# Kernel optimization log

Measured on AMD Instinct MI355X. Metric: run time of the kernel, lower is better.

## Reference

```python
import jax, jax.numpy as jnp
import numpy as np

B, T, A, F, K, DQ, DV = 64, 1024, 128, 1024, 31, 1024, 512  # filters F == T required by source math


def setup_inputs() -> dict:
    key = jax.random.key(0)
    ks = jax.random.split(key, 8)
    s = 0.05
    return {
        "query": jax.random.normal(ks[0], (B, 1, DQ), jnp.float32),
        "value": jax.random.normal(ks[1], (B, T, DV), jnp.float32),
        "attention_weights_cat": jax.random.uniform(ks[2], (B, T, 2), jnp.float32),
        "Wq": jax.random.normal(ks[3], (DQ, A), jnp.float32) * s,
        "Wm": jax.random.normal(ks[4], (DV, A), jnp.float32) * s,
        "Wv": jax.random.normal(ks[5], (A, 1), jnp.float32) * s,
        "Wconv": jax.random.normal(ks[6], (K, 2, F), jnp.float32) * s,
        "Wloc": jax.random.normal(ks[7], (T, A), jnp.float32) * s,
    }


def reference(query, value, attention_weights_cat, Wq, Wm, Wv, Wconv, Wloc):
    # query_layer: Dense(tanh, no bias): [B,1,DQ] -> [B,1,A]
    q = jnp.tanh(jnp.einsum('bld,da->bla', query, Wq))
    # memory_layer: Dense(tanh, no bias): [B,T,DV] -> [B,T,A]
    v = jnp.tanh(jnp.einsum('btd,da->bta', value, Wm))
    # location conv (SAME, no bias): [B,T,2] -> [B,T,F]
    loc = jax.lax.conv_general_dilated(
        attention_weights_cat, Wconv, window_strides=(1,), padding='SAME',
        dimension_numbers=('NWC', 'WIO', 'NWC'))
    # source transposes [0,2,1] then Dense(T->A, tanh): [B,F,T] -> [B,F,A]
    loc = jnp.tanh(jnp.einsum('bft,ta->bfa', jnp.transpose(loc, (0, 2, 1)), Wloc))
    # additive score (F == T so broadcast add is element-aligned): [B,T,1]
    score = jnp.einsum('bta,ao->bto', jnp.tanh(q + v + loc), Wv)
    alignment = jax.nn.softmax(score, axis=1)                # softmax over time
    context = jnp.sum(alignment * v, axis=1)                  # [B,A]
    return context, jnp.transpose(alignment, (0, 2, 1))       # [B,1,T]
```

## Files before the change

### kernel.cpp

```cpp
#include <hip/hip_runtime.h>
#include <hip/hip_bf16.h>

#define BB 64
#define TT 1024
#define AA 128
#define FF 1024
#define DQ 1024
#define DV 512

typedef __bf16 bf16x8_t __attribute__((ext_vector_type(8)));
typedef __bf16 bf16x4_t __attribute__((ext_vector_type(4)));
typedef float f32x4_t __attribute__((ext_vector_type(4)));
typedef _Float16 f16x4_t __attribute__((ext_vector_type(4)));

__device__ __forceinline__ float ftanh(float x) {
    float e = __expf(2.0f * x);
    return 1.0f - 2.0f / (e + 1.0f);
}

__device__ __forceinline__ __bf16 bhi(float x) { return (__bf16)x; }
__device__ __forceinline__ __bf16 blo(float x) {
    __bf16 h = (__bf16)x;
    return (__bf16)(x - (float)h);
}

__global__ __launch_bounds__(256) void k_prep(
    const float* __restrict__ Wm, const float* __restrict__ Wconv,
    const float* __restrict__ Wloc, const float* __restrict__ query,
    const float* __restrict__ Wq,
    __bf16* __restrict__ pwmhi, __bf16* __restrict__ pwmlo,
    __bf16* __restrict__ wcthi, __bf16* __restrict__ wctlo,
    __bf16* __restrict__ pwlhi, __bf16* __restrict__ pwllo,
    float* __restrict__ q_ws) {
    __shared__ float ls[128 * 65];
    int bx = blockIdx.x, tid = threadIdx.x;
    if (bx < 16) {
        int s = bx, d0 = s * 32;
        for (int i = tid; i < 4096; i += 256) {
            int dd = i >> 7, a = i & 127;
            ls[a * 33 + dd] = Wm[(d0 + dd) * AA + a];
        }
        __syncthreads();
#pragma unroll
        for (int u = 0; u < 2; u++) {
            int pos = tid * 2 + u;
            int l15 = pos & 15, lq = (pos >> 4) & 3, g = pos >> 6;
            bf16x8_t h8, l8;
#pragma unroll
            for (int j = 0; j < 8; j++) {
                float x = ls[(g * 16 + l15) * 33 + lq * 8 + j];
                h8[j] = bhi(x);
                l8[j] = blo(x);
            }
            size_t off = (size_t)(s * 512 + pos) * 8;
            *(bf16x8_t*)(pwmhi + off) = h8;
            *(bf16x8_t*)(pwmlo + off) = l8;
        }
    } else if (bx < 24) {
        int f0 = (bx - 16) * 128;
        for (int i = tid; i < 8192; i += 256) {
            int kc = i >> 7, f = i & 127;
            ls[f * 65 + kc] = (kc < 62) ? Wconv[kc * FF + f0 + f] : 0.f;
        }
        __syncthreads();
        int f = tid >> 1, half = tid & 1;
#pragma unroll
        for (int g = 0; g < 4; g++) {
            bf16x8_t h8, l8;
#pragma unroll
            for (int j = 0; j < 8; j++) {
                float x = ls[f * 65 + half * 32 + g * 8 + j];
                h8[j] = bhi(x);
                l8[j] = blo(x);
            }
            size_t off = (size_t)(f0 + f) * 64 + half * 32 + g * 8;
            *(bf16x8_t*)(wcthi + off) = h8;
            *(bf16x8_t*)(wctlo + off) = l8;
        }
    } else if (bx < 56) {
        int s2 = bx - 24, t0 = s2 * 32;
        for (int i = tid; i < 4096; i += 256) {
            int tt = i >> 7, a = i & 127;
            ls[a * 33 + tt] = Wloc[(t0 + tt) * AA + a];
        }
        __syncthreads();
#pragma unroll
        for (int u = 0; u < 2; u++) {
            int pos = tid * 2 + u;
            int l15 = pos & 15, lq = (pos >> 4) & 3, g = pos >> 6;
            bf16x8_t h8, l8;
#pragma unroll
            for (int j = 0; j < 8; j++) {
                float x = ls[(g * 16 + l15) * 33 + lq * 8 + j];
                h8[j] = bhi(x);
                l8[j] = blo(x);
            }
            size_t off = (size_t)(s2 * 512 + pos) * 8;
            *(bf16x8_t*)(pwlhi + off) = h8;
            *(bf16x8_t*)(pwllo + off) = l8;
        }
    } else {
        int b = bx - 56;
        int a = tid & 127, half = tid >> 7;
        const float* qrow = query + b * DQ + half * 512;
        float a0 = 0.f, a1 = 0.f, a2 = 0.f, a3 = 0.f;
        for (int d = 0; d < 512; d += 4) {
            float4 qv = *(const float4*)(qrow + d);
            int dg = (half * 512 + d) * AA + a;
            a0 += qv.x * Wq[dg];
            a1 += qv.y * Wq[dg + AA];
            a2 += qv.z * Wq[dg + 2 * AA];
            a3 += qv.w * Wq[dg + 3 * AA];
        }
        ls[tid] = a0 + a1 + a2 + a3;
        __syncthreads();
        if (half == 0) q_ws[b * AA + a] = ftanh(ls[a] + ls[a + 128]);
    }
}

__global__ __launch_bounds__(256) void k_zq(
    const float* __restrict__ xcat,
    const __bf16* __restrict__ pwlhi, const __bf16* __restrict__ pwllo,
    __bf16* __restrict__ zthi, __bf16* __restrict__ ztlo) {
    int b = blockIdx.x, tid = threadIdx.x;
    __shared__ float xs0[1056], xs1[1056];
    __shared__ float zs[64 * 132];
    for (int i = tid; i < 1056; i += 256) {
        int t = i - 16;
        float2 xv = (t >= 0 && t < TT) ? *(const float2*)(xcat + (size_t)(b * TT + t) * 2)
                                       : make_float2(0.f, 0.f);
        xs0[i] = xv.x;
        xs1[i] = xv.y;
    }
    __syncthreads();
    int lane = tid & 63, wid = tid >> 6;
    int wm = wid >> 1, wn = wid & 1;
    int l15 = lane & 15, lq = lane >> 4;

    f32x4_t zacc[2][4];
#pragma unroll
    for (int mi = 0; mi < 2; mi++)
#pragma unroll
        for (int ni = 0; ni < 4; ni++) zacc[mi][ni] = (f32x4_t){0.f, 0.f, 0.f, 0.f};

    for (int s = 0; s < 32; s++) {
        int t0 = s * 32;
        bf16x8_t bh[4], bl[4];
#pragma unroll
        for (int ni = 0; ni < 4; ni++) {
            size_t poff = (size_t)((s * 8 + wn * 4 + ni) * 64 + lane) * 8;
            bh[ni] = *(const bf16x8_t*)(pwlhi + poff);
            bl[ni] = *(const bf16x8_t*)(pwllo + poff);
        }
        bf16x8_t ah[2], al[2];
#pragma unroll
        for (int mi = 0; mi < 2; mi++) {
            int kc = wm * 32 + mi * 16 + l15;
            const float* xsc = (kc & 1) ? xs1 : xs0;
            int base = t0 + lq * 8 + (kc >> 1) + 1;
#pragma unroll
            for (int j = 0; j < 8; j++) {
                float x = xsc[base + j];
                ah[mi][j] = bhi(x);
                al[mi][j] = blo(x);
            }
        }
#pragma unroll
        for (int ni = 0; ni < 4; ni++)
#pragma unroll
            for (int mi = 0; mi < 2; mi++) {
                zacc[mi][ni] = __builtin_amdgcn_mfma_f32_16x16x32_bf16(ah[mi], bh[ni], zacc[mi][ni], 0, 0, 0);
                zacc[mi][ni] = __builtin_amdgcn_mfma_f32_16x16x32_bf16(al[mi], bh[ni], zacc[mi][ni], 0, 0, 0);
                zacc[mi][ni] = __builtin_amdgcn_mfma_f32_16x16x32_bf16(ah[mi], bl[ni], zacc[mi][ni], 0, 0, 0);
            }
    }
#pragma unroll
    for (int mi = 0; mi < 2; mi++)
#pragma unroll
        for (int ni = 0; ni < 4; ni++)
#pragma unroll
            for (int r = 0; r < 4; r++)
                zs[(wm * 32 + mi * 16 + lq * 4 + r) * 132 + wn * 64 + ni * 16 + l15] = zacc[mi][ni][r];
    __syncthreads();
    int a = tid >> 1, half = tid & 1;
#pragma unroll
    for (int g = 0; g < 4; g++) {
        bf16x8_t h8, l8;
#pragma unroll
        for (int j = 0; j < 8; j++) {
            float x = zs[(half * 32 + g * 8 + j) * 132 + a];
            h8[j] = bhi(x);
            l8[j] = blo(x);
        }
        size_t off = ((size_t)b * AA + a) * 64 + half * 32 + g * 8;
        *(bf16x8_t*)(zthi + off) = h8;
        *(bf16x8_t*)(ztlo + off) = l8;
    }
}

__global__ __launch_bounds__(256) void k_main(
    const float* __restrict__ value,
    const __bf16* __restrict__ pwmhi, const __bf16* __restrict__ pwmlo,
    const __bf16* __restrict__ wcthi, const __bf16* __restrict__ wctlo,
    const __bf16* __restrict__ zthi, const __bf16* __restrict__ ztlo,
    const float* __restrict__ q_ws, const float* __restrict__ Wv,
    _Float16* __restrict__ v_ws, float* __restrict__ score) {
    int b = blockIdx.x >> 3;
    int trow0 = (blockIdx.x & 7) << 7;
    int tid = threadIdx.x;
    int lane = tid & 63, wid = tid >> 6;
    int wm = wid >> 1, wn = wid & 1;
    int l15 = lane & 15, lq = lane >> 4;

    __shared__ __bf16 as_hi[128 * 40];
    __shared__ __bf16 as_lo[128 * 40];
    __shared__ float sc_red[256];

    f32x4_t acc[4][4];
#pragma unroll
    for (int mi = 0; mi < 4; mi++)
#pragma unroll
        for (int ni = 0; ni < 4; ni++) acc[mi][ni] = (f32x4_t){0.f, 0.f, 0.f, 0.f};

    const float* vbase = value + (size_t)(b * TT + trow0) * DV;
    int t0r = tid >> 3, c4 = tid & 7;
    float4 cur[4];
#pragma unroll
    for (int l = 0; l < 4; l++)
        cur[l] = *(const float4*)(vbase + (size_t)(t0r + 32 * l) * DV + c4 * 4);

    for (int it = 0; it < 16; ++it) {
        int d0 = it * 32;
        bf16x8_t bh[4], bl[4];
#pragma unroll
        for (int ni = 0; ni < 4; ni++) {
            size_t poff = (size_t)((it * 8 + wn * 4 + ni) * 64 + lane) * 8;
            bh[ni] = *(const bf16x8_t*)(pwmhi + poff);
            bl[ni] = *(const bf16x8_t*)(pwmlo + poff);
        }
        __syncthreads();
#pragma unroll
        for (int l = 0; l < 4; l++) {
            int t = t0r + 32 * l;
            float4 v4 = cur[l];
            bf16x4_t hv, lv;
            hv[0] = bhi(v4.x); lv[0] = blo(v4.x);
            hv[1] = bhi(v4.y); lv[1] = blo(v4.y);
            hv[2] = bhi(v4.z); lv[2] = blo(v4.z);
            hv[3] = bhi(v4.w); lv[3] = blo(v4.w);
            *(bf16x4_t*)(as_hi + t * 40 + c4 * 4) = hv;
            *(bf16x4_t*)(as_lo + t * 40 + c4 * 4) = lv;
        }
        __syncthreads();
        if (it < 15) {
#pragma unroll
            for (int l = 0; l < 4; l++)
                cur[l] = *(const float4*)(vbase + (size_t)(t0r + 32 * l) * DV + d0 + 32 + c4 * 4);
        }
        bf16x8_t ah[4], al[4];
#pragma unroll
        for (int mi = 0; mi < 4; mi++) {
            int off2 = (wm * 64 + mi * 16 + l15) * 40 + lq * 8;
            ah[mi] = *(const bf16x8_t*)(as_hi + off2);
            al[mi] = *(const bf16x8_t*)(as_lo + off2);
        }
#pragma unroll
        for (int mi = 0; mi < 4; mi++)
#pragma unroll
            for (int ni = 0; ni < 4; ni++) {
                acc[mi][ni] = __builtin_amdgcn_mfma_f32_16x16x32_bf16(ah[mi], bh[ni], acc[mi][ni], 0, 0, 0);
                acc[mi][ni] = __builtin_amdgcn_mfma_f32_16x16x32_bf16(al[mi], bh[ni], acc[mi][ni], 0, 0, 0);
                acc[mi][ni] = __builtin_amdgcn_mfma_f32_16x16x32_bf16(ah[mi], bl[ni], acc[mi][ni], 0, 0, 0);
            }
    }

    f32x4_t lacc[4][4];
#pragma unroll
    for (int mi = 0; mi < 4; mi++)
#pragma unroll
        for (int ni = 0; ni < 4; ni++) lacc[mi][ni] = (f32x4_t){0.f, 0.f, 0.f, 0.f};
#pragma unroll
    for (int kc0 = 0; kc0 < 64; kc0 += 32) {
        bf16x8_t a2h[4], a2l[4], b2h[4], b2l[4];
#pragma unroll
        for (int mi = 0; mi < 4; mi++) {
            int f = trow0 + wm * 64 + mi * 16 + l15;
            a2h[mi] = *(const bf16x8_t*)(wcthi + (size_t)f * 64 + kc0 + lq * 8);
            a2l[mi] = *(const bf16x8_t*)(wctlo + (size_t)f * 64 + kc0 + lq * 8);
        }
#pragma unroll
        for (int ni = 0; ni < 4; ni++) {
            int a = wn * 64 + ni * 16 + l15;
            size_t off = ((size_t)b * AA + a) * 64 + kc0 + lq * 8;
            b2h[ni] = *(const bf16x8_t*)(zthi + off);
            b2l[ni] = *(const bf16x8_t*)(ztlo + off);
        }
#pragma unroll
        for (int mi = 0; mi < 4; mi++)
#pragma unroll
            for (int ni = 0; ni < 4; ni++) {
                lacc[mi][ni] = __builtin_amdgcn_mfma_f32_16x16x32_bf16(a2h[mi], b2h[ni], lacc[mi][ni], 0, 0, 0);
                lacc[mi][ni] = __builtin_amdgcn_mfma_f32_16x16x32_bf16(a2l[mi], b2h[ni], lacc[mi][ni], 0, 0, 0);
                lacc[mi][ni] = __builtin_amdgcn_mfma_f32_16x16x32_bf16(a2h[mi], b2l[ni], lacc[mi][ni], 0, 0, 0);
            }
    }

    float qv[4], wv[4];
#pragma unroll
    for (int ni = 0; ni < 4; ni++) {
        int a = wn * 64 + ni * 16 + l15;
        qv[ni] = q_ws[b * AA + a];
        wv[ni] = Wv[a];
    }
#pragma unroll
    for (int mi = 0; mi < 4; mi++) {
#pragma unroll
        for (int r = 0; r < 4; r++) {
            int tl = wm * 64 + mi * 16 + lq * 4 + r;
            int t = trow0 + tl;
            float s = 0.f;
#pragma unroll
            for (int ni = 0; ni < 4; ni++) {
                float v = ftanh(acc[mi][ni][r]);
                float loc = ftanh(lacc[mi][ni][r]);
                int a = wn * 64 + ni * 16 + l15;
                v_ws[(size_t)(b * TT + t) * AA + a] = (_Float16)v;
                s += ftanh(qv[ni] + v + loc) * wv[ni];
            }
            s += __shfl_xor(s, 1, 64);
            s += __shfl_xor(s, 2, 64);
            s += __shfl_xor(s, 4, 64);
            s += __shfl_xor(s, 8, 64);
            if (l15 == 0) sc_red[wn * 128 + tl] = s;
        }
    }
    __syncthreads();
    if (tid < 128) score[b * TT + trow0 + tid] = sc_red[tid] + sc_red[128 + tid];
}

__global__ void k_softmax(const float* __restrict__ score, float* __restrict__ out_align) {
    int b = blockIdx.x, tid = threadIdx.x;
    __shared__ float red[4];
    float s[4];
#pragma unroll
    for (int i = 0; i < 4; i++) s[i] = score[b * TT + tid + i * 256];
    float m = fmaxf(fmaxf(s[0], s[1]), fmaxf(s[2], s[3]));
    for (int off = 32; off; off >>= 1) m = fmaxf(m, __shfl_xor(m, off, 64));
    int wid = tid >> 6;
    if ((tid & 63) == 0) red[wid] = m;
    __syncthreads();
    float M = fmaxf(fmaxf(red[0], red[1]), fmaxf(red[2], red[3]));
    __syncthreads();
    float e[4];
    float sum = 0.f;
#pragma unroll
    for (int i = 0; i < 4; i++) { e[i] = __expf(s[i] - M); sum += e[i]; }
    for (int off = 32; off; off >>= 1) sum += __shfl_xor(sum, off, 64);
    if ((tid & 63) == 0) red[wid] = sum;
    __syncthreads();
    float inv = 1.0f / (red[0] + red[1] + red[2] + red[3]);
#pragma unroll
    for (int i = 0; i < 4; i++) out_align[b * TT + tid + i * 256] = e[i] * inv;
}

__global__ void k_context(const float* __restrict__ align, const _Float16* __restrict__ v_ws,
                          float* __restrict__ out_ctx) {
    int b = blockIdx.y, t0 = blockIdx.x * 64, tid = threadIdx.x;
    int a0 = (tid & 31) * 4, tl = tid >> 5;
    __shared__ float sh[8 * 132];
    f32x4_t acc = (f32x4_t){0.f, 0.f, 0.f, 0.f};
    for (int tt = tl; tt < 64; tt += 8) {
        float w = align[b * TT + t0 + tt];
        f16x4_t vv = *(const f16x4_t*)(v_ws + (size_t)(b * TT + t0 + tt) * AA + a0);
        acc[0] += w * (float)vv[0];
        acc[1] += w * (float)vv[1];
        acc[2] += w * (float)vv[2];
        acc[3] += w * (float)vv[3];
    }
    *(f32x4_t*)&sh[tl * 132 + a0] = acc;
    __syncthreads();
    if (tid < 128) {
        float s = 0.f;
#pragma unroll
        for (int j = 0; j < 8; j++) s += sh[j * 132 + tid];
        atomicAdd(out_ctx + b * AA + tid, s);
    }
}

extern "C" void kernel_launch(void* const* d_in, const int* in_sizes, int n_in,
                              void* d_out, int out_size, void* d_ws, size_t ws_size,
                              hipStream_t stream) {
    const float* query = (const float*)d_in[0];
    const float* value = (const float*)d_in[1];
    const float* xcat  = (const float*)d_in[2];
    const float* Wq    = (const float*)d_in[3];
    const float* Wm    = (const float*)d_in[4];
    const float* Wv    = (const float*)d_in[5];
    const float* Wconv = (const float*)d_in[6];
    const float* Wloc  = (const float*)d_in[7];
    float* out = (float*)d_out;

    float* ws = (float*)d_ws;
    float* q_ws  = ws;
    float* sc_ws = q_ws + 8192;
    _Float16* v_ws = (_Float16*)(sc_ws + 65536);
    __bf16* pwmhi = (__bf16*)(sc_ws + 65536 + 4194304);
    __bf16* pwmlo = pwmhi + 65536;
    __bf16* wcthi = pwmlo + 65536;
    __bf16* wctlo = wcthi + 65536;
    __bf16* pwlhi = wctlo + 65536;
    __bf16* pwllo = pwlhi + 131072;
    __bf16* zthi  = pwllo + 131072;
    __bf16* ztlo  = zthi + 524288;

    (void)hipMemsetAsync(out, 0, (size_t)8192 * 4, stream);

    k_prep<<<120, 256, 0, stream>>>(Wm, Wconv, Wloc, query, Wq,
                                    pwmhi, pwmlo, wcthi, wctlo, pwlhi, pwllo, q_ws);
    k_zq<<<BB, 256, 0, stream>>>(xcat, pwlhi, pwllo, zthi, ztlo);
    k_main<<<512, 256, 0, stream>>>(value, pwmhi, pwmlo, wcthi, wctlo, zthi, ztlo,
                                    q_ws, Wv, v_ws, sc_ws);
    k_softmax<<<BB, 256, 0, stream>>>(sc_ws, out + 8192);
    k_context<<<dim3(16, BB), 256, 0, stream>>>(out + 8192, v_ws, out);
}
```

Measured before the change: 294.5 us.

## Merge prep kernels, halve main tile with double-buffered LDS, fuse softmax and context

The Wloc repacking and z computation move into a single pre-kernel that loads Wloc tiles straight into LDS, and the query projection is spread over more blocks. The main kernel halves its row tile to 64, launches twice as many blocks, double-buffers the value tile in LDS with one barrier per iteration, and reads conv and z operands pre-packed in MFMA fragment order. Softmax and the context reduction are fused into one kernel that writes directly, removing the memset and the atomics. Each z block now rereads Wloc per step, and the smaller tiles reload more packed weights per output row.

```diff
diff --git a/kernel.cpp b/kernel.cpp
--- a/kernel.cpp
+++ b/kernel.cpp
@@ -4,35 +4,32 @@
 #define BB 64
 #define TT 1024
 #define AA 128
-#define FF 1024
 #define DQ 1024
 #define DV 512
 
 typedef __bf16 bf16x8_t __attribute__((ext_vector_type(8)));
 typedef __bf16 bf16x4_t __attribute__((ext_vector_type(4)));
 typedef float f32x4_t __attribute__((ext_vector_type(4)));
-typedef _Float16 f16x4_t __attribute__((ext_vector_type(4)));
 
 __device__ __forceinline__ float ftanh(float x) {
     float e = __expf(2.0f * x);
     return 1.0f - 2.0f / (e + 1.0f);
 }
-
 __device__ __forceinline__ __bf16 bhi(float x) { return (__bf16)x; }
 __device__ __forceinline__ __bf16 blo(float x) {
     __bf16 h = (__bf16)x;
     return (__bf16)(x - (float)h);
 }
 
-__global__ __launch_bounds__(256) void k_prep(
+__global__ __launch_bounds__(256) void k_pre(
     const float* __restrict__ Wm, const float* __restrict__ Wconv,
     const float* __restrict__ Wloc, const float* __restrict__ query,
-    const float* __restrict__ Wq,
+    const float* __restrict__ Wq, const float* __restrict__ xcat,
     __bf16* __restrict__ pwmhi, __bf16* __restrict__ pwmlo,
-    __bf16* __restrict__ wcthi, __bf16* __restrict__ wctlo,
-    __bf16* __restrict__ pwlhi, __bf16* __restrict__ pwllo,
+    __bf16* __restrict__ pwchi, __bf16* __restrict__ pwclo,
+    __bf16* __restrict__ pzhi, __bf16* __restrict__ pzlo,
     float* __restrict__ q_ws) {
-    __shared__ float ls[128 * 65];
+    __shared__ float ls[14784];
     int bx = blockIdx.x, tid = threadIdx.x;
     if (bx < 16) {
         int s = bx, d0 = s * 32;
@@ -60,177 +57,190 @@
         int f0 = (bx - 16) * 128;
         for (int i = tid; i < 8192; i += 256) {
             int kc = i >> 7, f = i & 127;
-            ls[f * 65 + kc] = (kc < 62) ? Wconv[kc * FF + f0 + f] : 0.f;
-        }
-        __syncthreads();
-        int f = tid >> 1, half = tid & 1;
-#pragma unroll
-        for (int g = 0; g < 4; g++) {
+            ls[f * 65 + kc] = (kc < 62) ? Wconv[kc * 1024 + f0 + f] : 0.f;
+        }
+        __syncthreads();
+#pragma unroll
+        for (int u = 0; u < 4; u++) {
+            int pos = tid * 4 + u;
+            int fg = pos >> 7, kq = (pos >> 6) & 1, ln = pos & 63;
+            int l15 = ln & 15, lq = ln >> 4;
             bf16x8_t h8, l8;
 #pragma unroll
             for (int j = 0; j < 8; j++) {
-                float x = ls[f * 65 + half * 32 + g * 8 + j];
+                float x = ls[(fg * 16 + l15) * 65 + kq * 32 + lq * 8 + j];
                 h8[j] = bhi(x);
                 l8[j] = blo(x);
             }
-            size_t off = (size_t)(f0 + f) * 64 + half * 32 + g * 8;
-            *(bf16x8_t*)(wcthi + off) = h8;
-            *(bf16x8_t*)(wctlo + off) = l8;
-        }
-    } else if (bx < 56) {
-        int s2 = bx - 24, t0 = s2 * 32;
-        for (int i = tid; i < 4096; i += 256) {
-            int tt = i >> 7, a = i & 127;
-            ls[a * 33 + tt] = Wloc[(t0 + tt) * AA + a];
-        }
-        __syncthreads();
-#pragma unroll
-        for (int u = 0; u < 2; u++) {
-            int pos = tid * 2 + u;
-            int l15 = pos & 15, lq = (pos >> 4) & 3, g = pos >> 6;
+            size_t off = ((size_t)(((bx - 16) * 8 + fg) * 2 + kq) * 64 + ln) * 8;
+            *(bf16x8_t*)(pwchi + off) = h8;
+            *(bf16x8_t*)(pwclo + off) = l8;
+        }
+    } else if (bx < 280) {
+        int bidx = bx - 24;
+        int b = bidx >> 2, ag = bidx & 3;
+        int lane32 = tid & 31, grp = tid >> 5;
+        int a = ag * 32 + lane32;
+        float acc = 0.f;
+        const float* qrow = query + b * DQ + grp * 128;
+        const float* wqb = Wq + (size_t)grp * 128 * AA + a;
+        for (int d = 0; d < 128; d += 4) {
+            float4 q4 = *(const float4*)(qrow + d);
+            acc += q4.x * wqb[d * AA] + q4.y * wqb[(d + 1) * AA] +
+                   q4.z * wqb[(d + 2) * AA] + q4.w * wqb[(d + 3) * AA];
+        }
+        ls[grp * 33 + lane32] = acc;
+        __syncthreads();
+        if (tid < 32) {
+            float s = 0.f;
+#pragma unroll
+            for (int j = 0; j < 8; j++) s += ls[j * 33 + tid];
+            q_ws[b * AA + ag * 32 + tid] = ftanh(s);
+        }
+    } else {
+        int b = bx - 280;
+        float* xs0 = ls;
+        float* xs1 = ls + 1056;
+        float* wl = ls + 2112;
+        float* zs = ls + 6336;
+        for (int i = tid; i < 1056; i += 256) {
+            int t = i - 16;
+            float2 xv = (t >= 0 && t < TT) ? *(const float2*)(xcat + (size_t)(b * TT + t) * 2)
+                                           : make_float2(0.f, 0.f);
+            xs0[i] = xv.x;
+            xs1[i] = xv.y;
+        }
+        int lane = tid & 63, wid = tid >> 6;
+        int wm = wid >> 1, wn = wid & 1;
+        int l15 = lane & 15, lq = lane >> 4;
+        f32x4_t zacc[2][4];
+#pragma unroll
+        for (int mi = 0; mi < 2; mi++)
+#pragma unroll
+            for (int ni = 0; ni < 4; ni++) zacc[mi][ni] = (f32x4_t){0.f, 0.f, 0.f, 0.f};
+        for (int s = 0; s < 32; s++) {
+            int t0 = s * 32;
+            __syncthreads();
+#pragma unroll
+            for (int k2 = 0; k2 < 4; k2++) {
+                int slot = tid + k2 * 256;
+                int tt = slot >> 5, c4 = slot & 31;
+                *(float4*)(wl + tt * 132 + c4 * 4) =
+                    *(const float4*)(Wloc + (size_t)(t0 + tt) * AA + c4 * 4);
+            }
+            __syncthreads();
+            bf16x8_t ah[2], al[2];
+#pragma unroll
+            for (int mi = 0; mi < 2; mi++) {
+                int kc = wm * 32 + mi * 16 + l15;
+                const float* xsc = (kc & 1) ? xs1 : xs0;
+                int base = t0 + lq * 8 + (kc >> 1) + 1;
+#pragma unroll
+                for (int j = 0; j < 8; j++) {
+                    float x = xsc[base + j];
+                    ah[mi][j] = bhi(x);
+                    al[mi][j] = blo(x);
+                }
+            }
+#pragma unroll
+            for (int ni = 0; ni < 4; ni++) {
+                int a = wn * 64 + ni * 16 + l15;
+                bf16x8_t bh, bl;
+#pragma unroll
+                for (int j = 0; j < 8; j++) {
+                    float x = wl[(lq * 8 + j) * 132 + a];
+                    bh[j] = bhi(x);
+                    bl[j] = blo(x);
+                }
+#pragma unroll
+                for (int mi = 0; mi < 2; mi++) {
+                    zacc[mi][ni] = __builtin_amdgcn_mfma_f32_16x16x32_bf16(ah[mi], bh, zacc[mi][ni], 0, 0, 0);
+                    zacc[mi][ni] = __builtin_amdgcn_mfma_f32_16x16x32_bf16(al[mi], bh, zacc[mi][ni], 0, 0, 0);
+                    zacc[mi][ni] = __builtin_amdgcn_mfma_f32_16x16x32_bf16(ah[mi], bl, zacc[mi][ni], 0, 0, 0);
+                }
+            }
+        }
+        __syncthreads();
+#pragma unroll
+        for (int mi = 0; mi < 2; mi++)
+#pragma unroll
+            for (int ni = 0; ni < 4; ni++)
+#pragma unroll
+                for (int r = 0; r < 4; r++)
+                    zs[(wm * 32 + mi * 16 + lq * 4 + r) * 132 + wn * 64 + ni * 16 + l15] = zacc[mi][ni][r];
+        __syncthreads();
+#pragma unroll
+        for (int u = 0; u < 4; u++) {
+            int pos = tid * 4 + u;
+            int a16 = pos >> 7, kq = (pos >> 6) & 1, ln = pos & 63;
+            int pl15 = ln & 15, plq = ln >> 4;
             bf16x8_t h8, l8;
 #pragma unroll
             for (int j = 0; j < 8; j++) {
-                float x = ls[(g * 16 + l15) * 33 + lq * 8 + j];
+                float x = zs[(kq * 32 + plq * 8 + j) * 132 + a16 * 16 + pl15];
                 h8[j] = bhi(x);
                 l8[j] = blo(x);
             }
-            size_t off = (size_t)(s2 * 512 + pos) * 8;
-            *(bf16x8_t*)(pwlhi + off) = h8;
-            *(bf16x8_t*)(pwllo + off) = l8;
-        }
-    } else {
-        int b = bx - 56;
-        int a = tid & 127, half = tid >> 7;
-        const float* qrow = query + b * DQ + half * 512;
-        float a0 = 0.f, a1 = 0.f, a2 = 0.f, a3 = 0.f;
-        for (int d = 0; d < 512; d += 4) {
-            float4 qv = *(const float4*)(qrow + d);
-            int dg = (half * 512 + d) * AA + a;
-            a0 += qv.x * Wq[dg];
-            a1 += qv.y * Wq[dg + AA];
-            a2 += qv.z * Wq[dg + 2 * AA];
-            a3 += qv.w * Wq[dg + 3 * AA];
-        }
-        ls[tid] = a0 + a1 + a2 + a3;
-        __syncthreads();
-        if (half == 0) q_ws[b * AA + a] = ftanh(ls[a] + ls[a + 128]);
-    }
-}
-
-__global__ __launch_bounds__(256) void k_zq(
-    const float* __restrict__ xcat,
-    const __bf16* __restrict__ pwlhi, const __bf16* __restrict__ pwllo,
-    __bf16* __restrict__ zthi, __bf16* __restrict__ ztlo) {
-    int b = blockIdx.x, tid = threadIdx.x;
-    __shared__ float xs0[1056], xs1[1056];
-    __shared__ float zs[64 * 132];
-    for (int i = tid; i < 1056; i += 256) {
-        int t = i - 16;
-        float2 xv = (t >= 0 && t < TT) ? *(const float2*)(xcat + (size_t)(b * TT + t) * 2)
-                                       : make_float2(0.f, 0.f);
-        xs0[i] = xv.x;
-        xs1[i] = xv.y;
-    }
-    __syncthreads();
-    int lane = tid & 63, wid = tid >> 6;
-    int wm = wid >> 1, wn = wid & 1;
-    int l15 = lane & 15, lq = lane >> 4;
-
-    f32x4_t zacc[2][4];
-#pragma unroll
-    for (int mi = 0; mi < 2; mi++)
-#pragma unroll
-        for (int ni = 0; ni < 4; ni++) zacc[mi][ni] = (f32x4_t){0.f, 0.f, 0.f, 0.f};
-
-    for (int s = 0; s < 32; s++) {
-        int t0 = s * 32;
-        bf16x8_t bh[4], bl[4];
-#pragma unroll
-        for (int ni = 0; ni < 4; ni++) {
-            size_t poff = (size_t)((s * 8 + wn * 4 + ni) * 64 + lane) * 8;
-            bh[ni] = *(const bf16x8_t*)(pwlhi + poff);
-            bl[ni] = *(const bf16x8_t*)(pwllo + poff);
-        }
-        bf16x8_t ah[2], al[2];
-#pragma unroll
-        for (int mi = 0; mi < 2; mi++) {
-            int kc = wm * 32 + mi * 16 + l15;
-            const float* xsc = (kc & 1) ? xs1 : xs0;
-            int base = t0 + lq * 8 + (kc >> 1) + 1;
-#pragma unroll
-            for (int j = 0; j < 8; j++) {
-                float x = xsc[base + j];
-                ah[mi][j] = bhi(x);
-                al[mi][j] = blo(x);
-            }
-        }
-#pragma unroll
-        for (int ni = 0; ni < 4; ni++)
-#pragma unroll
-            for (int mi = 0; mi < 2; mi++) {
-                zacc[mi][ni] = __builtin_amdgcn_mfma_f32_16x16x32_bf16(ah[mi], bh[ni], zacc[mi][ni], 0, 0, 0);
-                zacc[mi][ni] = __builtin_amdgcn_mfma_f32_16x16x32_bf16(al[mi], bh[ni], zacc[mi][ni], 0, 0, 0);
-                zacc[mi][ni] = __builtin_amdgcn_mfma_f32_16x16x32_bf16(ah[mi], bl[ni], zacc[mi][ni], 0, 0, 0);
-            }
-    }
-#pragma unroll
-    for (int mi = 0; mi < 2; mi++)
-#pragma unroll
-        for (int ni = 0; ni < 4; ni++)
-#pragma unroll
-            for (int r = 0; r < 4; r++)
-                zs[(wm * 32 + mi * 16 + lq * 4 + r) * 132 + wn * 64 + ni * 16 + l15] = zacc[mi][ni][r];
-    __syncthreads();
-    int a = tid >> 1, half = tid & 1;
-#pragma unroll
-    for (int g = 0; g < 4; g++) {
-        bf16x8_t h8, l8;
-#pragma unroll
-        for (int j = 0; j < 8; j++) {
-            float x = zs[(half * 32 + g * 8 + j) * 132 + a];
-            h8[j] = bhi(x);
-            l8[j] = blo(x);
-        }
-        size_t off = ((size_t)b * AA + a) * 64 + half * 32 + g * 8;
-        *(bf16x8_t*)(zthi + off) = h8;
-        *(bf16x8_t*)(ztlo + off) = l8;
+            size_t off = (((size_t)b * 16 + a16 * 2 + kq) * 64 + ln) * 8;
+            *(bf16x8_t*)(pzhi + off) = h8;
+            *(bf16x8_t*)(pzlo + off) = l8;
+        }
     }
 }
 
 __global__ __launch_bounds__(256) void k_main(
     const float* __restrict__ value,
     const __bf16* __restrict__ pwmhi, const __bf16* __restrict__ pwmlo,
-    const __bf16* __restrict__ wcthi, const __bf16* __restrict__ wctlo,
-    const __bf16* __restrict__ zthi, const __bf16* __restrict__ ztlo,
+    const __bf16* __restrict__ pwchi, const __bf16* __restrict__ pwclo,
+    const __bf16* __restrict__ pzhi, const __bf16* __restrict__ pzlo,
     const float* __restrict__ q_ws, const float* __restrict__ Wv,
     _Float16* __restrict__ v_ws, float* __restrict__ score) {
-    int b = blockIdx.x >> 3;
-    int trow0 = (blockIdx.x & 7) << 7;
+    int b = blockIdx.x >> 4;
+    int trow0 = (blockIdx.x & 15) << 6;
     int tid = threadIdx.x;
     int lane = tid & 63, wid = tid >> 6;
     int wm = wid >> 1, wn = wid & 1;
     int l15 = lane & 15, lq = lane >> 4;
 
-    __shared__ __bf16 as_hi[128 * 40];
-    __shared__ __bf16 as_lo[128 * 40];
-    __shared__ float sc_red[256];
-
-    f32x4_t acc[4][4];
-#pragma unroll
-    for (int mi = 0; mi < 4; mi++)
+    __shared__ __bf16 as_hi[2][64 * 40];
+    __shared__ __bf16 as_lo[2][64 * 40];
+    __shared__ float sc_red[128];
+
+    f32x4_t acc[2][4];
+#pragma unroll
+    for (int mi = 0; mi < 2; mi++)
 #pragma unroll
         for (int ni = 0; ni < 4; ni++) acc[mi][ni] = (f32x4_t){0.f, 0.f, 0.f, 0.f};
 
     const float* vbase = value + (size_t)(b * TT + trow0) * DV;
-    int t0r = tid >> 3, c4 = tid & 7;
-    float4 cur[4];
-#pragma unroll
-    for (int l = 0; l < 4; l++)
-        cur[l] = *(const float4*)(vbase + (size_t)(t0r + 32 * l) * DV + c4 * 4);
+    int row0 = tid >> 3, c4 = tid & 7;
+    float4 cur0[2], cur1[2];
+#pragma unroll
+    for (int l = 0; l < 2; l++) {
+        int slot = tid + l * 256;
+        cur0[l] = *(const float4*)(vbase + (size_t)(slot >> 3) * DV + 0 + (slot & 7) * 4);
+    }
+#pragma unroll
+    for (int l = 0; l < 2; l++) {
+        int slot = tid + l * 256;
+        cur1[l] = *(const float4*)(vbase + (size_t)(slot >> 3) * DV + 32 + (slot & 7) * 4);
+    }
+#pragma unroll
+    for (int l = 0; l < 2; l++) {
+        int slot = tid + l * 256;
+        int t = slot >> 3, cc = slot & 7;
+        float4 v4 = cur0[l];
+        bf16x4_t hv, lv;
+        hv[0] = bhi(v4.x); lv[0] = blo(v4.x);
+        hv[1] = bhi(v4.y); lv[1] = blo(v4.y);
+        hv[2] = bhi(v4.z); lv[2] = blo(v4.z);
+        hv[3] = bhi(v4.w); lv[3] = blo(v4.w);
+        *(bf16x4_t*)(&as_hi[0][t * 40 + cc * 4]) = hv;
+        *(bf16x4_t*)(&as_lo[0][t * 40 + cc * 4]) = lv;
+    }
 
     for (int it = 0; it < 16; ++it) {
-        int d0 = it * 32;
+        __syncthreads();
         bf16x8_t bh[4], bl[4];
 #pragma unroll
         for (int ni = 0; ni < 4; ni++) {
@@ -238,65 +248,71 @@
             bh[ni] = *(const bf16x8_t*)(pwmhi + poff);
             bl[ni] = *(const bf16x8_t*)(pwmlo + poff);
         }
-        __syncthreads();
-#pragma unroll
-        for (int l = 0; l < 4; l++) {
-            int t = t0r + 32 * l;
-            float4 v4 = cur[l];
-            bf16x4_t hv, lv;
-            hv[0] = bhi(v4.x); lv[0] = blo(v4.x);
-            hv[1] = bhi(v4.y); lv[1] = blo(v4.y);
-            hv[2] = bhi(v4.z); lv[2] = blo(v4.z);
-            hv[3] = bhi(v4.w); lv[3] = blo(v4.w);
-            *(bf16x4_t*)(as_hi + t * 40 + c4 * 4) = hv;
-            *(bf16x4_t*)(as_lo + t * 40 + c4 * 4) = lv;
-        }
-        __syncthreads();
+        int nb = (it + 1) & 1;
         if (it < 15) {
 #pragma unroll
-            for (int l = 0; l < 4; l++)
-                cur[l] = *(const float4*)(vbase + (size_t)(t0r + 32 * l) * DV + d0 + 32 + c4 * 4);
-        }
-        bf16x8_t ah[4], al[4];
-#pragma unroll
-        for (int mi = 0; mi < 4; mi++) {
-            int off2 = (wm * 64 + mi * 16 + l15) * 40 + lq * 8;
-            ah[mi] = *(const bf16x8_t*)(as_hi + off2);
-            al[mi] = *(const bf16x8_t*)(as_lo + off2);
-        }
-#pragma unroll
-        for (int mi = 0; mi < 4; mi++)
-#pragma unroll
-            for (int ni = 0; ni < 4; ni++) {
+            for (int l = 0; l < 2; l++) {
+                int slot = tid + l * 256;
+                int t = slot >> 3, cc = slot & 7;
+                float4 v4 = nb ? cur1[l] : cur0[l];
+                bf16x4_t hv, lv;
+                hv[0] = bhi(v4.x); lv[0] = blo(v4.x);
+                hv[1] = bhi(v4.y); lv[1] = blo(v4.y);
+                hv[2] = bhi(v4.z); lv[2] = blo(v4.z);
+                hv[3] = bhi(v4.w); lv[3] = blo(v4.w);
+                *(bf16x4_t*)(&as_hi[nb][t * 40 + cc * 4]) = hv;
+                *(bf16x4_t*)(&as_lo[nb][t * 40 + cc * 4]) = lv;
+            }
+        }
+        if (it < 14) {
+#pragma unroll
+            for (int l = 0; l < 2; l++) {
+                int slot = tid + l * 256;
+                float4 v4 = *(const float4*)(vbase + (size_t)(slot >> 3) * DV + (it + 2) * 32 + (slot & 7) * 4);
+                if (it & 1) cur1[l] = v4; else cur0[l] = v4;
+            }
+        }
+        int cb = it & 1;
+        bf16x8_t ah[2], al[2];
+#pragma unroll
+        for (int mi = 0; mi < 2; mi++) {
+            int off2 = (wm * 32 + mi * 16 + l15) * 40 + lq * 8;
+            ah[mi] = *(const bf16x8_t*)(&as_hi[cb][off2]);
+            al[mi] = *(const bf16x8_t*)(&as_lo[cb][off2]);
+        }
+#pragma unroll
+        for (int ni = 0; ni < 4; ni++)
+#pragma unroll
+            for (int mi = 0; mi < 2; mi++) {
                 acc[mi][ni] = __builtin_amdgcn_mfma_f32_16x16x32_bf16(ah[mi], bh[ni], acc[mi][ni], 0, 0, 0);
                 acc[mi][ni] = __builtin_amdgcn_mfma_f32_16x16x32_bf16(al[mi], bh[ni], acc[mi][ni], 0, 0, 0);
                 acc[mi][ni] = __builtin_amdgcn_mfma_f32_16x16x32_bf16(ah[mi], bl[ni], acc[mi][ni], 0, 0, 0);
             }
     }
 
-    f32x4_t lacc[4][4];
-#pragma unroll
-    for (int mi = 0; mi < 4; mi++)
+    f32x4_t lacc[2][4];
+#pragma unroll
+    for (int mi = 0; mi < 2; mi++)
 #pragma unroll
         for (int ni = 0; ni < 4; ni++) lacc[mi][ni] = (f32x4_t){0.f, 0.f, 0.f, 0.f};
 #pragma unroll
-    for (int kc0 = 0; kc0 < 64; kc0 += 32) {
-        bf16x8_t a2h[4], a2l[4], b2h[4], b2l[4];
-#pragma unroll
-        for (int mi = 0; mi < 4; mi++) {
-            int f = trow0 + wm * 64 + mi * 16 + l15;
-            a2h[mi] = *(const bf16x8_t*)(wcthi + (size_t)f * 64 + kc0 + lq * 8);
-            a2l[mi] = *(const bf16x8_t*)(wctlo + (size_t)f * 64 + kc0 + lq * 8);
+    for (int kq = 0; kq < 2; kq++) {
+        bf16x8_t a2h[2], a2l[2], b2h[4], b2l[4];
+#pragma unroll
+        for (int mi = 0; mi < 2; mi++) {
+            int fg = (trow0 >> 4) + wm * 2 + mi;
+            size_t off = ((size_t)(fg * 2 + kq) * 64 + lane) * 8;
+            a2h[mi] = *(const bf16x8_t*)(pwchi + off);
+            a2l[mi] = *(const bf16x8_t*)(pwclo + off);
         }
 #pragma unroll
         for (int ni = 0; ni < 4; ni++) {
-            int a = wn * 64 + ni * 16 + l15;
-            size_t off = ((size_t)b * AA + a) * 64 + kc0 + lq * 8;
-            b2h[ni] = *(const bf16x8_t*)(zthi + off);
-            b2l[ni] = *(const bf16x8_t*)(ztlo + off);
-        }
-#pragma unroll
-        for (int mi = 0; mi < 4; mi++)
+            size_t off = (((size_t)b * 16 + (wn * 4 + ni) * 2 + kq) * 64 + lane) * 8;
+            b2h[ni] = *(const bf16x8_t*)(pzhi + off);
+            b2l[ni] = *(const bf16x8_t*)(pzlo + off);
+        }
+#pragma unroll
+        for (int mi = 0; mi < 2; mi++)
 #pragma unroll
             for (int ni = 0; ni < 4; ni++) {
                 lacc[mi][ni] = __builtin_amdgcn_mfma_f32_16x16x32_bf16(a2h[mi], b2h[ni], lacc[mi][ni], 0, 0, 0);
@@ -313,10 +329,10 @@
         wv[ni] = Wv[a];
     }
 #pragma unroll
-    for (int mi = 0; mi < 4; mi++) {
+    for (int mi = 0; mi < 2; mi++) {
 #pragma unroll
         for (int r = 0; r < 4; r++) {
-            int tl = wm * 64 + mi * 16 + lq * 4 + r;
+            int tl = wm * 32 + mi * 16 + lq * 4 + r;
             int t = trow0 + tl;
             float s = 0.f;
 #pragma unroll
@@ -331,60 +347,61 @@
             s += __shfl_xor(s, 2, 64);
             s += __shfl_xor(s, 4, 64);
             s += __shfl_xor(s, 8, 64);
-            if (l15 == 0) sc_red[wn * 128 + tl] = s;
+            if (l15 == 0) sc_red[wn * 64 + tl] = s;
         }
     }
     __syncthreads();
-    if (tid < 128) score[b * TT + trow0 + tid] = sc_red[tid] + sc_red[128 + tid];
-}
-
-__global__ void k_softmax(const float* __restrict__ score, float* __restrict__ out_align) {
-    int b = blockIdx.x, tid = threadIdx.x;
+    if (tid < 64) score[b * TT + trow0 + tid] = sc_red[tid] + sc_red[64 + tid];
+}
+
+__global__ __launch_bounds__(256) void k_post(const float* __restrict__ score,
+                                              const _Float16* __restrict__ v_ws,
+                                              float* __restrict__ out) {
+    int h = blockIdx.x & 1, b = blockIdx.x >> 1;
+    int tid = threadIdx.x;
+    __shared__ float sc[1024];
     __shared__ float red[4];
+    __shared__ float part[4][72];
     float s[4];
 #pragma unroll
     for (int i = 0; i < 4; i++) s[i] = score[b * TT + tid + i * 256];
     float m = fmaxf(fmaxf(s[0], s[1]), fmaxf(s[2], s[3]));
     for (int off = 32; off; off >>= 1) m = fmaxf(m, __shfl_xor(m, off, 64));
-    int wid = tid >> 6;
-    if ((tid & 63) == 0) red[wid] = m;
+    int wd = tid >> 6;
+    if ((tid & 63) == 0) red[wd] = m;
     __syncthreads();
     float M = fmaxf(fmaxf(red[0], red[1]), fmaxf(red[2], red[3]));
     __syncthreads();
-    float e[4];
     float sum = 0.f;
 #pragma unroll
-    for (int i = 0; i < 4; i++) { e[i] = __expf(s[i] - M); sum += e[i]; }
+    for (int i = 0; i < 4; i++) {
+        float e = __expf(s[i] - M);
+        sc[tid + i * 256] = e;
+        sum += e;
+    }
     for (int off = 32; off; off >>= 1) sum += __shfl_xor(sum, off, 64);
-    if ((tid & 63) == 0) red[wid] = sum;
+    if ((tid & 63) == 0) red[wd] = sum;
     __syncthreads();
     float inv = 1.0f / (red[0] + red[1] + red[2] + red[3]);
-#pragma unroll
-    for (int i = 0; i < 4; i++) out_align[b * TT + tid + i * 256] = e[i] * inv;
-}
-
-__global__ void k_context(const float* __restrict__ align, const _Float16* __restrict__ v_ws,
-                          float* __restrict__ out_ctx) {
-    int b = blockIdx.y, t0 = blockIdx.x * 64, tid = threadIdx.x;
-    int a0 = (tid & 31) * 4, tl = tid >> 5;
-    __shared__ float sh[8 * 132];
-    f32x4_t acc = (f32x4_t){0.f, 0.f, 0.f, 0.f};
-    for (int tt = tl; tt < 64; tt += 8) {
-        float w = align[b * TT + t0 + tt];
-        f16x4_t vv = *(const f16x4_t*)(v_ws + (size_t)(b * TT + t0 + tt) * AA + a0);
-        acc[0] += w * (float)vv[0];
-        acc[1] += w * (float)vv[1];
-        acc[2] += w * (float)vv[2];
-        acc[3] += w * (float)vv[3];
-    }
-    *(f32x4_t*)&sh[tl * 132 + a0] = acc;
+    float* align_out = out + 8192 + b * TT;
+#pragma unroll
+    for (int i = 0; i < 2; i++) {
+        int t = h * 512 + tid + i * 256;
+        align_out[t] = sc[t] * inv;
+    }
+    int al = tid & 63, tg = tid >> 6;
+    const _Float16* vb = v_ws + (size_t)b * TT * AA + h * 64 + al;
+    float a0 = 0.f, a1 = 0.f, a2 = 0.f, a3 = 0.f;
+    for (int t = tg * 4; t < TT; t += 16) {
+        a0 += sc[t + 0] * (float)vb[(size_t)(t + 0) * AA];
+        a1 += sc[t + 1] * (float)vb[(size_t)(t + 1) * AA];
+        a2 += sc[t + 2] * (float)vb[(size_t)(t + 2) * AA];
+        a3 += sc[t + 3] * (float)vb[(size_t)(t + 3) * AA];
+    }
+    part[tg][al] = (a0 + a1 + a2 + a3) * inv;
     __syncthreads();
-    if (tid < 128) {
-        float s = 0.f;
-#pragma unroll
-        for (int j = 0; j < 8; j++) s += sh[j * 132 + tid];
-        atomicAdd(out_ctx + b * AA + tid, s);
-    }
+    if (tid < 64)
+        out[b * AA + h * 64 + tid] = part[0][tid] + part[1][tid] + part[2][tid] + part[3][tid];
 }
 
 extern "C" void kernel_launch(void* const* d_in, const int* in_sizes, int n_in,
@@ -402,24 +419,18 @@
 
     float* ws = (float*)d_ws;
     float* q_ws  = ws;
-    float* sc_ws = q_ws + 8192;
-    _Float16* v_ws = (_Float16*)(sc_ws + 65536);
-    __bf16* pwmhi = (__bf16*)(sc_ws + 65536 + 4194304);
+    float* sc_ws = ws + 8192;
+    _Float16* v_ws = (_Float16*)(ws + 8192 + 65536);
+    __bf16* pwmhi = (__bf16*)(ws + 8192 + 65536 + 4194304);
     __bf16* pwmlo = pwmhi + 65536;
-    __bf16* wcthi = pwmlo + 65536;
-    __bf16* wctlo = wcthi + 65536;
-    __bf16* pwlhi = wctlo + 65536;
-    __bf16* pwllo = pwlhi + 131072;
-    __bf16* zthi  = pwllo + 131072;
-    __bf16* ztlo  = zthi + 524288;
-
-    (void)hipMemsetAsync(out, 0, (size_t)8192 * 4, stream);
-
-    k_prep<<<120, 256, 0, stream>>>(Wm, Wconv, Wloc, query, Wq,
-                                    pwmhi, pwmlo, wcthi, wctlo, pwlhi, pwllo, q_ws);
-    k_zq<<<BB, 256, 0, stream>>>(xcat, pwlhi, pwllo, zthi, ztlo);
-    k_main<<<512, 256, 0, stream>>>(value, pwmhi, pwmlo, wcthi, wctlo, zthi, ztlo,
-                                    q_ws, Wv, v_ws, sc_ws);
-    k_softmax<<<BB, 256, 0, stream>>>(sc_ws, out + 8192);
-    k_context<<<dim3(16, BB), 256, 0, stream>>>(out + 8192, v_ws, out);
-}
+    __bf16* pwchi = pwmlo + 65536;
+    __bf16* pwclo = pwchi + 65536;
+    __bf16* pzhi  = pwclo + 65536;
+    __bf16* pzlo  = pzhi + 524288;
+
+    k_pre<<<344, 256, 0, stream>>>(Wm, Wconv, Wloc, query, Wq, xcat,
+                                   pwmhi, pwmlo, pwchi, pwclo, pzhi, pzlo, q_ws);
+    k_main<<<1024, 256, 0, stream>>>(value, pwmhi, pwmlo, pwchi, pwclo, pzhi, pzlo,
+                                     q_ws, Wv, v_ws, sc_ws);
+    k_post<<<128, 256, 0, stream>>>(sc_ws, v_ws, out);
+}
```

After: 306.7 us. 4.1% more time.
